# Optimization experiments

Measured on AMD Instinct MI355X. Metric: run time of the kernel, lower is better.

Reference implementation:

```python
import jax, jax.numpy as jnp
import numpy as np

B, T, D, V, N = 64, 512, 256, 32000, 48


def gru_layer(x_tbd, wx, wh, b):
    """Keras GRU (reset_after=True). x_tbd: [T,B,Din]; returns [T,B,D]."""
    bx, bh = b[0], b[1]
    px = x_tbd @ wx + bx  # [T,B,3D] precomputed input projections
    units = wh.shape[0]

    def step(h, pxt):
        ph = h @ wh + bh
        xz, xr, xh = jnp.split(pxt, 3, axis=-1)
        hz, hr, hh = jnp.split(ph, 3, axis=-1)
        z = jax.nn.sigmoid(xz + hz)
        r = jax.nn.sigmoid(xr + hr)
        hc = jnp.tanh(xh + r * hh)
        hn = z * h + (1.0 - z) * hc
        return hn, hn

    h0 = jnp.zeros((x_tbd.shape[1], units), x_tbd.dtype)
    _, out = jax.lax.scan(step, h0, px)
    return out


def crf_log_likelihood(emis, tags, seq_len, trans):
    Bb, Tt, Nn = emis.shape
    t_idx = jnp.arange(Tt)
    mask = (t_idx[None, :] < seq_len[:, None]).astype(emis.dtype)  # [B,T]
    unary = jnp.take_along_axis(emis, tags[..., None], axis=2)[..., 0]
    us = jnp.sum(unary * mask, axis=1)
    tr = trans[tags[:, :-1], tags[:, 1:]]  # [B,T-1]
    ts = jnp.sum(tr * mask[:, 1:], axis=1)

    def step(alpha, inp):
        e_t, m_t = inp  # [B,N], [B]
        new = jax.nn.logsumexp(alpha[:, :, None] + trans[None], axis=1) + e_t
        return jnp.where(m_t[:, None], new, alpha), None

    alpha, _ = jax.lax.scan(step, emis[:, 0],
                            (emis.transpose(1, 0, 2)[1:], (mask > 0).T[1:]))
    log_z = jax.nn.logsumexp(alpha, axis=-1)
    return us + ts - log_z


def crf_decode(emis, trans, seq_len):
    Bb, Tt, Nn = emis.shape
    mask = jnp.arange(Tt)[None, :] < seq_len[:, None]
    ident = jnp.arange(Nn, dtype=jnp.int32)[None, :]

    def step(alpha, inp):
        e_t, m_t = inp
        sc = alpha[:, :, None] + trans[None]  # [B,N,N] prev->cur
        bp = jnp.argmax(sc, axis=1).astype(jnp.int32)
        new = jnp.max(sc, axis=1) + e_t
        alpha_n = jnp.where(m_t[:, None], new, alpha)
        bp = jnp.where(m_t[:, None], bp, ident)
        return alpha_n, bp

    alpha, bps = jax.lax.scan(step, emis[:, 0],
                              (emis.transpose(1, 0, 2)[1:], mask.T[1:]))
    score = jnp.max(alpha, axis=-1)
    last = jnp.argmax(alpha, axis=-1).astype(jnp.int32)  # [B]

    def back(tag, bp):
        prev = jnp.take_along_axis(bp, tag[:, None], axis=1)[:, 0]
        return prev, tag

    tag0, tags = jax.lax.scan(back, last, bps, reverse=True)  # tags[i]=pos i+1
    pred = jnp.concatenate([tag0[:, None], tags.T], axis=1)  # [B,T]
    return pred, score


def setup_inputs() -> dict:
    key = jax.random.key(0)
    ks = jax.random.split(key, 20)
    s = 0.05
    inp = {
        'x': jax.random.randint(ks[0], (B, T), 0, V, dtype=jnp.int32),
        'y': jax.random.randint(ks[1], (B, T), 0, N, dtype=jnp.int32),
        'seq_len': jax.random.randint(ks[2], (B,), T // 2, T + 1, dtype=jnp.int32),
        'embed': jax.random.normal(ks[3], (V, D), jnp.float32) * s,
        'wx_f': jax.random.normal(ks[4], (D, 3 * D), jnp.float32) * s,
        'wh_f': jax.random.normal(ks[5], (D, 3 * D), jnp.float32) * s,
        'b_f': jnp.zeros((2, 3 * D), jnp.float32),
        'wx_b': jax.random.normal(ks[6], (D, 3 * D), jnp.float32) * s,
        'wh_b': jax.random.normal(ks[7], (D, 3 * D), jnp.float32) * s,
        'b_b': jnp.zeros((2, 3 * D), jnp.float32),
        'wq': jax.random.normal(ks[8], (2 * D, D), jnp.float32) * s,
        'bq': jnp.zeros((D,), jnp.float32),
        'wk': jax.random.normal(ks[9], (2 * D, D), jnp.float32) * s,
        'bk': jnp.zeros((D,), jnp.float32),
        'wv': jax.random.normal(ks[10], (2 * D, D), jnp.float32) * s,
        'bv': jnp.zeros((D,), jnp.float32),
        'wt': jax.random.normal(ks[11], (D, N), jnp.float32) * s,
        'bt': jnp.zeros((N,), jnp.float32),
        'trans': jax.random.normal(ks[12], (N, N), jnp.float32) * s,
    }
    return inp


def reference(x, y, seq_len, embed, wx_f, wh_f, b_f, wx_b, wh_b, b_b,
              wq, bq, wk, bk, wv, bv, wt, bt, trans):
    emb = embed[x]  # [B,T,D]
    xt = emb.transpose(1, 0, 2)  # [T,B,D]
    hf = gru_layer(xt, wx_f, wh_f, b_f)
    hb = gru_layer(xt[::-1], wx_b, wh_b, b_b)[::-1]
    h = jnp.concatenate([hf, hb], axis=-1).transpose(1, 0, 2)  # [B,T,2D]
    q = h @ wq + bq
    k = h @ wk + bk
    v = h @ wv + bv
    w = jax.nn.softmax(jnp.einsum('btd,bsd->bts', q, k), axis=-1)
    a = jnp.einsum('bts,bsd->btd', w, v)
    logits = a @ wt + bt  # [B,T,N]
    pred, _ = crf_decode(logits, trans, seq_len)
    ll = crf_log_likelihood(logits, y, seq_len, trans)
    return pred, ll
```

## Files before the change

### kernel.cpp

```cpp
#include <hip/hip_runtime.h>
#include <math.h>

typedef float f32;
typedef short short8 __attribute__((ext_vector_type(8)));
typedef float f32x4 __attribute__((ext_vector_type(4)));

#define TT 512
#define BB 64
#define DD 256
#define NN 48

static const size_t OFF_EBF  = 0;
static const size_t OFF_PXF  = 16384000;
static const size_t OFF_PXB  = OFF_PXF + 50331648;
static const size_t OFF_HBF_F= OFF_PXB + 50331648;
static const size_t OFF_HBF_B= OFF_HBF_F + 16777216;
static const size_t OFF_WXTF = OFF_HBF_B + 16777216;
static const size_t OFF_WXTB = OFF_WXTF + 393216;
static const size_t OFF_WHTF = OFF_WXTB + 393216;
static const size_t OFF_WHTB = OFF_WHTF + 393216;
static const size_t OFF_WQT  = OFF_WHTB + 393216;
static const size_t OFF_WKT  = OFF_WQT + 262144;
static const size_t OFF_WVT  = OFF_WKT + 262144;
static const size_t OFF_WTT  = OFF_WVT + 262144;
static const size_t OFF_QBF = OFF_PXF;
static const size_t OFF_KBF = OFF_QBF + 16777216;
static const size_t OFF_VBF = OFF_KBF + 16777216;
static const size_t OFF_VT  = OFF_VBF + 16777216;
static const size_t OFF_SCB = OFF_VT  + 16777216;
static const size_t OFF_ABF = OFF_QBF;
static const size_t OFF_LG  = OFF_KBF;

__device__ __forceinline__ ushort f2bf(f32 f) {
  union { f32 f; unsigned u; } v; v.f = f;
  unsigned r = v.u + 0x7fffu + ((v.u >> 16) & 1u);
  return (ushort)(r >> 16);
}
__device__ __forceinline__ f32 bf2f(ushort u) {
  union { unsigned u; f32 f; } v; v.u = ((unsigned)u) << 16; return v.f;
}
__device__ __forceinline__ f32 fsigmoid(f32 x) { return 1.f / (1.f + __expf(-x)); }
__device__ __forceinline__ f32 ftanh(f32 x) { return 1.f - 2.f / (__expf(2.f * x) + 1.f); }

template <int PL2>
__global__ __launch_bounds__(256) void tconv_k(
    const f32* __restrict__ in, ushort* __restrict__ out, int total, int Q) {
  int o = blockIdx.x * 256 + threadIdx.x;
  if (o >= total) return;
  int q = o >> PL2, p = o & ((1 << PL2) - 1);
  out[o] = f2bf(in[(size_t)p * Q + q]);
}

__global__ __launch_bounds__(256) void conv_embed_k(
    const f32* __restrict__ in, ushort* __restrict__ out, int n4) {
  int i = blockIdx.x * 256 + threadIdx.x;
  if (i >= n4) return;
  float4 v = ((const float4*)in)[i];
  ushort4 o;
  o.x = f2bf(v.x); o.y = f2bf(v.y); o.z = f2bf(v.z); o.w = f2bf(v.w);
  ((ushort4*)out)[i] = o;
}

__global__ __launch_bounds__(256) void tr_v_k(
    const ushort* __restrict__ in, ushort* __restrict__ out) {
  __shared__ ushort tile[32][33];
  int b = blockIdx.z;
  int s0 = blockIdx.x * 32, d0 = blockIdx.y * 32;
  int xc = threadIdx.x & 31, y0 = threadIdx.x >> 5;
  for (int yy = y0; yy < 32; yy += 8)
    tile[yy][xc] = in[((size_t)b * 512 + s0 + yy) * 256 + d0 + xc];
  __syncthreads();
  for (int yy = y0; yy < 32; yy += 8)
    out[((size_t)b * 256 + d0 + yy) * 512 + s0 + xc] = tile[xc][yy];
}

enum { GM_PX = 0, GM_QKV = 1, GM_SC = 2, GM_AV = 3, GM_LG = 4 };

template <int MODE>
__global__ __launch_bounds__(256) void mgemm(
    const ushort* __restrict__ Aa, const ushort* __restrict__ Ab,
    const ushort* __restrict__ Bt,
    f32* __restrict__ Cf, ushort* __restrict__ Cb,
    const f32* __restrict__ bias, const int* __restrict__ xi,
    int Ndim, int K, int rev) {
  const int m0 = blockIdx.y * 128;
  const int n0 = blockIdx.x * 128;
  const int bz = blockIdx.z;
  const int tid = threadIdx.x;
  const int l = tid & 63, w = tid >> 6;
  const int wr = w >> 1, wc = w & 1;
  __shared__ __align__(16) short Al[128 * 40];
  __shared__ __align__(16) short Bl[128 * 40];
  f32x4 acc[4][4] = {};

  const int rowa = tid >> 1;
  const int kha = (tid & 1) * 16;
  const int rA = m0 + rowa;
  const ushort* aBase = nullptr;
  const ushort* aBase2 = nullptr;
  if constexpr (MODE == GM_PX) {
    int tg = rA >> 6, b = rA & 63;
    int ts = rev ? (511 - tg) : tg;
    aBase = Aa + (size_t)xi[b * 512 + ts] * 256;
  } else if constexpr (MODE == GM_QKV) {
    int bl = rA >> 9, t = rA & 511;
    aBase = Aa + ((size_t)(t * 64 + bl)) * 256;
    aBase2 = Ab + ((size_t)((511 - t) * 64 + bl)) * 256;
  } else if constexpr (MODE == GM_SC) {
    aBase = Aa + ((size_t)(bz * 512 + rA)) * 256;
  } else if constexpr (MODE == GM_AV) {
    aBase = Aa + ((size_t)(bz * 512 + rA)) * 512;
  } else {
    aBase = Aa + (size_t)rA * 256;
  }
  const int rowb = tid >> 1;
  const int khb = (tid & 1) * 16;
  int rowg = n0 + rowb;
  if constexpr (MODE == GM_SC) rowg += bz * 512;
  if constexpr (MODE == GM_AV) rowg += bz * 256;
  const ushort* bBase = Bt + (size_t)rowg * K;
  const bool bValid = (MODE != GM_LG) || (n0 + rowb < Ndim);

  for (int k0 = 0; k0 < K; k0 += 32) {
    {
      int kk = k0 + kha;
      const ushort* src;
      if constexpr (MODE == GM_QKV)
        src = (kk < 256) ? aBase + kk : aBase2 + (kk - 256);
      else
        src = aBase + kk;
      uint4 a0 = *(const uint4*)src;
      uint4 a1 = *(const uint4*)(src + 8);
      *(uint4*)&Al[rowa * 40 + kha] = a0;
      *(uint4*)&Al[rowa * 40 + kha + 8] = a1;
    }
    {
      uint4 v0 = make_uint4(0, 0, 0, 0), v1 = make_uint4(0, 0, 0, 0);
      if (bValid) {
        const ushort* src = bBase + k0 + khb;
        v0 = *(const uint4*)src;
        v1 = *(const uint4*)(src + 8);
      }
      *(uint4*)&Bl[rowb * 40 + khb] = v0;
      *(uint4*)&Bl[rowb * 40 + khb + 8] = v1;
    }
    __syncthreads();
    const int fr = l & 15, fg = l >> 4;
    short8 af[4], bfr[4];
#pragma unroll
    for (int mf = 0; mf < 4; ++mf)
      af[mf] = *(const short8*)&Al[(wr * 64 + mf * 16 + fr) * 40 + fg * 8];
#pragma unroll
    for (int nf = 0; nf < 4; ++nf)
      bfr[nf] = *(const short8*)&Bl[(wc * 64 + nf * 16 + fr) * 40 + fg * 8];
#pragma unroll
    for (int mf = 0; mf < 4; ++mf)
#pragma unroll
      for (int nf = 0; nf < 4; ++nf)
        acc[mf][nf] = __builtin_amdgcn_mfma_f32_16x16x32_bf16(
            af[mf], bfr[nf], acc[mf][nf], 0, 0, 0);
    __syncthreads();
  }

  const int fr = l & 15, fq = l >> 4;
#pragma unroll
  for (int mf = 0; mf < 4; ++mf) {
#pragma unroll
    for (int nf = 0; nf < 4; ++nf) {
      int col = n0 + wc * 64 + nf * 16 + fr;
      f32 bs = 0.f;
      if (bias && col < Ndim) bs = bias[col];
#pragma unroll
      for (int rg = 0; rg < 4; ++rg) {
        int row = m0 + wr * 64 + mf * 16 + fq * 4 + rg;
        f32 vv = acc[mf][nf][rg] + bs;
        if constexpr (MODE == GM_PX) {
          int tg = row >> 6, b = row & 63;
          int gate = col >> 8, hc = col & 255;
          int rg4b = b >> 4, lr = b & 15;
          size_t idx = (size_t)tg * 49152 + (size_t)rg4b * 12288 +
                       (size_t)gate * 4096 + (size_t)(hc >> 4) * 256 +
                       (hc & 15) * 16 + (lr >> 2) * 4 + (lr & 3);
          Cb[idx] = f2bf(vv);
        } else if constexpr (MODE == GM_QKV)
          Cb[(size_t)row * 256 + col] = f2bf(vv);
        else if constexpr (MODE == GM_SC)
          Cb[((size_t)bz * 512 + row) * 512 + col] = f2bf(vv);
        else if constexpr (MODE == GM_AV)
          Cb[((size_t)bz * 512 + row) * 256 + col] = f2bf(vv);
        else {
          if (col < Ndim) Cf[(size_t)row * 48 + col] = vv;
        }
      }
    }
  }
}

#define MFMA_B16 __builtin_amdgcn_mfma_f32_16x16x32_bf16

#define PXLOAD(T, P) {                                         \
  size_t tb_ = (size_t)(T) * 49152;                            \
  P##0 = *(const uint2*)(px + tb_ + offp);                     \
  P##1 = *(const uint2*)(px + tb_ + offp + 4096);              \
  P##2 = *(const uint2*)(px + tb_ + offp + 8192);              \
}

#define GATE1(RI, UZ, UR, UH)                                  \
{                                                              \
  f32 zv_ = fsigmoid(az[RI] + bhz + bf2f((ushort)(UZ)));       \
  f32 rv_ = fsigmoid(ar[RI] + bhr + bf2f((ushort)(UR)));       \
  f32 hc_ = ftanh(bf2f((ushort)(UH)) + rv_ * (ah[RI] + bhh));  \
  f32 hn_ = zv_ * h0##RI + (1.f - zv_) * hc_;                  \
  h0##RI = hn_;                                                \
  *(ushort*)&dst_[(kb0 * 16 + fq * 4 + (RI)) * 16 + e2] = f2bf(hn_); \
}

#define STEP(T, BUF, PC, PN) {                                 \
  if ((T) + 1 < TT) PXLOAD((T) + 1, PN);                       \
  if ((T) > 0) {                                               \
    uint2 v_ = *(const uint2*)&ldsH[BUF][(ckb * 16 + crow) * 16 + chalf * 8]; \
    *(uint2*)&hseq[(((size_t)(T) - 1) * 64 + rowbase + crow) * 256 + ckb * 8 + chalf * 4] = v_; \
  }                                                            \
  uint2 q0_ = PC##0, q1_ = PC##1, q2_ = PC##2;                 \
  f32x4 az = {}, ar = {}, ah = {};                             \
  _Pragma("unroll")                                            \
  for (int ks = 0; ks < 8; ++ks) {                             \
    short8 a_  = *(const short8*)&ldsH[BUF][((ks * 4 + fq) * 16 + fr) * 16]; \
    short8 wh8 = *(const short8*)&ldsWh[wcol * 512 + ((ks * 64 + fq * 16) ^ ((wcol & 7) << 6))]; \
    az = MFMA_B16(a_, wz[ks], az, 0, 0, 0);                    \
    ar = MFMA_B16(a_, wrg[ks], ar, 0, 0, 0);                   \
    ah = MFMA_B16(a_, wh8, ah, 0, 0, 0);                       \
  }                                                            \
  char* dst_ = ldsH[(BUF) ^ 1];                                \
  GATE1(0, q0_.x,       q1_.x,       q2_.x)                    \
  GATE1(1, q0_.x >> 16, q1_.x >> 16, q2_.x >> 16)              \
  GATE1(2, q0_.y,       q1_.y,       q2_.y)                    \
  GATE1(3, q0_.y >> 16, q1_.y >> 16, q2_.y >> 16)              \
  __syncthreads();                                             \
}

__global__ __launch_bounds__(1024, 4) void gru_scan8(
    const ushort* __restrict__ pxf, const ushort* __restrict__ pxb,
    const ushort* __restrict__ whtf, const ushort* __restrict__ whtb,
    const f32* __restrict__ b_f, const f32* __restrict__ b_b,
    ushort* __restrict__ hfbf, ushort* __restrict__ hbbf) {
  const int dir = blockIdx.x >> 2;
  const int rg4 = blockIdx.x & 3;
  const int tid = threadIdx.x;
  const int w = tid >> 6, l = tid & 63;
  const int fr = l & 15, fq = l >> 4;
  const ushort* pxd = dir ? pxb : pxf;
  const ushort* wht = dir ? whtb : whtf;
  const f32* bh = (dir ? b_b : b_f) + 768;
  ushort* hseq = dir ? hbbf : hfbf;

  __shared__ __align__(16) char ldsWh[131072];
  __shared__ __align__(16) char ldsH[2][8192];

#pragma unroll
  for (int i = 0; i < 8; ++i) {
    int idx = i * 1024 + tid;
    int col = idx >> 5, kc = idx & 31;
    uint4 v = *(const uint4*)&wht[(size_t)(512 + col) * 256 + kc * 8];
    *(uint4*)&ldsWh[col * 512 + ((kc * 16) ^ ((col & 7) << 6))] = v;
  }
  if (tid < 512) ((uint4*)ldsH[0])[tid] = make_uint4(0, 0, 0, 0);

  const int wcol = w * 16 + fr;
  short8 wz[8], wrg[8];
#pragma unroll
  for (int ks = 0; ks < 8; ++ks) {
    wz[ks]  = *(const short8*)&wht[(size_t)wcol * 256 + ks * 32 + fq * 8];
    wrg[ks] = *(const short8*)&wht[(size_t)(256 + wcol) * 256 + ks * 32 + fq * 8];
  }
  const f32 bhz = bh[wcol], bhr = bh[256 + wcol], bhh = bh[512 + wcol];
  f32 h00 = 0.f, h01 = 0.f, h02 = 0.f, h03 = 0.f;

  const ushort* px = pxd + (size_t)rg4 * 12288;
  const int offp = w * 256 + fr * 16 + fq * 4;
  const int rowbase = rg4 * 16;
  const int kb0 = wcol >> 3;
  const int e2 = (wcol & 7) * 2;
  const int ckb = (tid >> 1) >> 4;
  const int crow = (tid >> 1) & 15;
  const int chalf = tid & 1;

  uint2 pA0, pA1, pA2;
  uint2 pB0, pB1, pB2;
  PXLOAD(0, pA);
  __syncthreads();

#pragma unroll 1
  for (int t2 = 0; t2 < TT; t2 += 2) {
    STEP(t2, 0, pA, pB);
    STEP(t2 + 1, 1, pB, pA);
  }
  {
    uint2 v = *(const uint2*)&ldsH[0][(ckb * 16 + crow) * 16 + chalf * 8];
    *(uint2*)&hseq[((size_t)511 * 64 + rowbase + crow) * 256 + ckb * 8 + chalf * 4] = v;
  }
}

__global__ __launch_bounds__(256) void softmax_ip(ushort* __restrict__ p) {
  size_t row = blockIdx.x;
  uint* pr = (uint*)(p + row * 512);
  int tid = threadIdx.x;
  uint u = pr[tid];
  f32 v0 = bf2f((ushort)(u & 0xffff)), v1 = bf2f((ushort)(u >> 16));
  f32 m = fmaxf(v0, v1);
  for (int off = 32; off; off >>= 1) m = fmaxf(m, __shfl_xor(m, off));
  __shared__ f32 red[4];
  __shared__ f32 red2[4];
  if ((tid & 63) == 0) red[tid >> 6] = m;
  __syncthreads();
  m = fmaxf(fmaxf(red[0], red[1]), fmaxf(red[2], red[3]));
  f32 e0 = __expf(v0 - m), e1 = __expf(v1 - m);
  f32 s = e0 + e1;
  for (int off = 32; off; off >>= 1) s += __shfl_xor(s, off);
  if ((tid & 63) == 0) red2[tid >> 6] = s;
  __syncthreads();
  s = red2[0] + red2[1] + red2[2] + red2[3];
  f32 inv = 1.f / s;
  pr[tid] = (uint)f2bf(e0 * inv) | ((uint)f2bf(e1 * inv) << 16);
}

__global__ __launch_bounds__(64) void crf_ll_k(
    const f32* __restrict__ logits, const int* __restrict__ y,
    const int* __restrict__ seq_len, const f32* __restrict__ trans,
    f32* __restrict__ out) {
  const int b = blockIdx.x, tid = threadIdx.x;
  __shared__ f32 tr[NN * NN];
  for (int i = tid; i < NN * NN; i += 64) tr[i] = trans[i];
  const f32* em = logits + (size_t)b * TT * NN;
  const int L = seq_len[b];
  const bool act = tid < NN;
  f32 Ecol[NN];
#pragma unroll
  for (int i = 0; i < NN; ++i)
    Ecol[i] = act ? __expf(trans[i * NN + tid]) : 0.f;
  f32 alpha = act ? em[tid] : -1e30f;
  __syncthreads();
  for (int t = 1; t < L; ++t) {
    f32 m = alpha;
    for (int off = 32; off; off >>= 1) m = fmaxf(m, __shfl_xor(m, off));
    f32 e = __expf(alpha - m);
    f32 s = 0.f;
#pragma unroll
    for (int i = 0; i < NN; ++i) s += __shfl(e, i) * Ecol[i];
    if (act) alpha = m + __logf(s) + em[t * NN + tid];
  }
  f32 us = 0.f, ts = 0.f;
  for (int t = tid; t < TT; t += 64) {
    if (t < L) {
      us += em[t * NN + y[b * TT + t]];
      if (t >= 1) ts += tr[y[b * TT + t - 1] * NN + y[b * TT + t]];
    }
  }
  for (int off = 32; off; off >>= 1) { us += __shfl_xor(us, off); ts += __shfl_xor(ts, off); }
  f32 m = alpha;
  for (int off = 32; off; off >>= 1) m = fmaxf(m, __shfl_xor(m, off));
  f32 e = __expf(alpha - m);
  f32 s = e;
  for (int off = 32; off; off >>= 1) s += __shfl_xor(s, off);
  if (tid == 0) out[(size_t)BB * TT + b] = us + ts - (m + __logf(s));
}

__global__ __launch_bounds__(64) void crf_decode_k(
    const f32* __restrict__ logits, const int* __restrict__ seq_len,
    const f32* __restrict__ trans, f32* __restrict__ out) {
  const int b = blockIdx.x, tid = threadIdx.x;
  __shared__ f32 tr[NN][NN];
  __shared__ f32 al[2][NN];
  __shared__ unsigned char bp[TT - 1][NN];
  __shared__ unsigned char pr[TT];
  for (int i = tid; i < NN * NN; i += 64) tr[i / NN][i % NN] = trans[i];
  const f32* em = logits + (size_t)b * TT * NN;
  const int L = seq_len[b];
  if (tid < NN) al[0][tid] = em[tid];
  __syncthreads();
  int cur = 0;
  for (int t = 1; t < TT; ++t) {
    if (tid < NN) {
      if (t < L) {
        f32 m = -1e30f; int arg = 0;
        for (int i = 0; i < NN; ++i) {
          f32 v = al[cur][i] + tr[i][tid];
          if (v > m) { m = v; arg = i; }
        }
        al[cur ^ 1][tid] = m + em[t * NN + tid];
        bp[t - 1][tid] = (unsigned char)arg;
      } else {
        al[cur ^ 1][tid] = al[cur][tid];
        bp[t - 1][tid] = (unsigned char)tid;
      }
    }
    __syncthreads();
    cur ^= 1;
  }
  if (tid == 0) {
    f32 m = -1e30f; int last = 0;
    for (int i = 0; i < NN; ++i)
      if (al[cur][i] > m) { m = al[cur][i]; last = i; }
    int tag = last;
    for (int t = TT - 2; t >= 0; --t) { pr[t + 1] = (unsigned char)tag; tag = bp[t][tag]; }
    pr[0] = (unsigned char)tag;
  }
  __syncthreads();
  for (int t = tid; t < TT; t += 64)
    out[(size_t)b * TT + t] = (f32)pr[t];
}

extern "C" void kernel_launch(void* const* d_in, const int* in_sizes, int n_in,
                              void* d_out, int out_size, void* d_ws, size_t ws_size,
                              hipStream_t stream) {
  const int* x       = (const int*)d_in[0];
  const int* y       = (const int*)d_in[1];
  const int* seq_len = (const int*)d_in[2];
  const f32* embed   = (const f32*)d_in[3];
  const f32* wx_f    = (const f32*)d_in[4];
  const f32* wh_f    = (const f32*)d_in[5];
  const f32* b_f     = (const f32*)d_in[6];
  const f32* wx_b    = (const f32*)d_in[7];
  const f32* wh_b    = (const f32*)d_in[8];
  const f32* b_b     = (const f32*)d_in[9];
  const f32* wq      = (const f32*)d_in[10];
  const f32* bq      = (const f32*)d_in[11];
  const f32* wk      = (const f32*)d_in[12];
  const f32* bk      = (const f32*)d_in[13];
  const f32* wv      = (const f32*)d_in[14];
  const f32* bv      = (const f32*)d_in[15];
  const f32* wt      = (const f32*)d_in[16];
  const f32* bt      = (const f32*)d_in[17];
  const f32* trans   = (const f32*)d_in[18];
  f32* out = (f32*)d_out;

  char* ws = (char*)d_ws;
  ushort* ebf  = (ushort*)(ws + OFF_EBF);
  ushort* pxfb = (ushort*)(ws + OFF_PXF);
  ushort* pxbb = (ushort*)(ws + OFF_PXB);
  ushort* hfbf = (ushort*)(ws + OFF_HBF_F);
  ushort* hbbf = (ushort*)(ws + OFF_HBF_B);
  ushort* wxtf = (ushort*)(ws + OFF_WXTF);
  ushort* wxtb = (ushort*)(ws + OFF_WXTB);
  ushort* whtf = (ushort*)(ws + OFF_WHTF);
  ushort* whtb = (ushort*)(ws + OFF_WHTB);
  ushort* wqt  = (ushort*)(ws + OFF_WQT);
  ushort* wkt  = (ushort*)(ws + OFF_WKT);
  ushort* wvt  = (ushort*)(ws + OFF_WVT);
  ushort* wtt  = (ushort*)(ws + OFF_WTT);
  ushort* qbf = (ushort*)(ws + OFF_QBF);
  ushort* kbf = (ushort*)(ws + OFF_KBF);
  ushort* vbf = (ushort*)(ws + OFF_VBF);
  ushort* vT  = (ushort*)(ws + OFF_VT);
  ushort* scb = (ushort*)(ws + OFF_SCB);
  ushort* abf = (ushort*)(ws + OFF_ABF);
  f32*    lg  = (f32*)(ws + OFF_LG);

  conv_embed_k<<<8000, 256, 0, stream>>>(embed, ebf, 2048000);
  tconv_k<8><<<768, 256, 0, stream>>>(wx_f, wxtf, 196608, 768);
  tconv_k<8><<<768, 256, 0, stream>>>(wx_b, wxtb, 196608, 768);
  tconv_k<8><<<768, 256, 0, stream>>>(wh_f, whtf, 196608, 768);
  tconv_k<8><<<768, 256, 0, stream>>>(wh_b, whtb, 196608, 768);
  tconv_k<9><<<512, 256, 0, stream>>>(wq, wqt, 131072, 256);
  tconv_k<9><<<512, 256, 0, stream>>>(wk, wkt, 131072, 256);
  tconv_k<9><<<512, 256, 0, stream>>>(wv, wvt, 131072, 256);
  tconv_k<8><<<48, 256, 0, stream>>>(wt, wtt, 12288, 48);

  mgemm<GM_PX><<<dim3(6, 256), 256, 0, stream>>>(
      ebf, nullptr, wxtf, nullptr, pxfb, b_f, x, 768, 256, 0);
  mgemm<GM_PX><<<dim3(6, 256), 256, 0, stream>>>(
      ebf, nullptr, wxtb, nullptr, pxbb, b_b, x, 768, 256, 1);
  gru_scan8<<<8, 1024, 0, stream>>>(pxfb, pxbb, whtf, whtb, b_f, b_b, hfbf, hbbf);

  mgemm<GM_QKV><<<dim3(2, 256), 256, 0, stream>>>(
      hfbf, hbbf, wqt, nullptr, qbf, bq, nullptr, 256, 512, 0);
  mgemm<GM_QKV><<<dim3(2, 256), 256, 0, stream>>>(
      hfbf, hbbf, wkt, nullptr, kbf, bk, nullptr, 256, 512, 0);
  mgemm<GM_QKV><<<dim3(2, 256), 256, 0, stream>>>(
      hfbf, hbbf, wvt, nullptr, vbf, bv, nullptr, 256, 512, 0);
  tr_v_k<<<dim3(16, 8, 64), 256, 0, stream>>>(vbf, vT);
  mgemm<GM_SC><<<dim3(4, 4, 64), 256, 0, stream>>>(
      qbf, nullptr, kbf, nullptr, scb, nullptr, nullptr, 512, 256, 0);
  softmax_ip<<<BB * TT, 256, 0, stream>>>(scb);
  mgemm<GM_AV><<<dim3(2, 4, 64), 256, 0, stream>>>(
      scb, nullptr, vT, nullptr, abf, nullptr, nullptr, 256, 512, 0);
  mgemm<GM_LG><<<dim3(1, 256), 256, 0, stream>>>(
      abf, nullptr, wtt, lg, nullptr, bt, nullptr, 48, 256, 0);

  crf_ll_k<<<BB, 64, 0, stream>>>(lg, y, seq_len, trans, out);
  crf_decode_k<<<BB, 64, 0, stream>>>(lg, seq_len, trans, out);
}
```

Baseline: 2.755 ms.

## Keep all GRU recurrent weights in registers with 512-thread scan blocks

The GRU scan kernel drops from 1024 to 512 threads per block, and each wave now covers two 16-column tiles. All three gate weight slices (z, r, h) are held in registers, which removes the 128KB LDS copy of the candidate-gate weights and its per-step LDS reads. The input-projection layout written by the PX GEMM is reordered so each thread loads one 16-byte vector per gate, and the h-sequence writeback uses 16-byte stores. The old one-step-ahead prefetch of projections is removed. This raises register pressure and halves the wave count available to hide latency in the serial recurrence.

```diff
diff --git a/kernel.cpp b/kernel.cpp
--- a/kernel.cpp
+++ b/kernel.cpp
@@ -177,10 +177,11 @@
         if constexpr (MODE == GM_PX) {
           int tg = row >> 6, b = row & 63;
           int gate = col >> 8, hc = col & 255;
+          int wv2 = hc >> 5, ctb2 = (hc >> 4) & 1, frb = hc & 15;
           int rg4b = b >> 4, lr = b & 15;
           size_t idx = (size_t)tg * 49152 + (size_t)rg4b * 12288 +
-                       (size_t)gate * 4096 + (size_t)(hc >> 4) * 256 +
-                       (hc & 15) * 16 + (lr >> 2) * 4 + (lr & 3);
+                       (size_t)gate * 4096 + (size_t)wv2 * 512 +
+                       frb * 32 + (lr >> 2) * 8 + ctb2 * 4 + (lr & 3);
           Cb[idx] = f2bf(vv);
         } else if constexpr (MODE == GM_QKV)
           Cb[(size_t)row * 256 + col] = f2bf(vv);
@@ -198,48 +199,49 @@
 
 #define MFMA_B16 __builtin_amdgcn_mfma_f32_16x16x32_bf16
 
-#define PXLOAD(T, P) {                                         \
-  size_t tb_ = (size_t)(T) * 49152;                            \
-  P##0 = *(const uint2*)(px + tb_ + offp);                     \
-  P##1 = *(const uint2*)(px + tb_ + offp + 4096);              \
-  P##2 = *(const uint2*)(px + tb_ + offp + 8192);              \
-}
-
-#define GATE1(RI, UZ, UR, UH)                                  \
+#define GATE1(CT, RI, UZ, UR, UH, AZ, AR, AH, KB)              \
 {                                                              \
-  f32 zv_ = fsigmoid(az[RI] + bhz + bf2f((ushort)(UZ)));       \
-  f32 rv_ = fsigmoid(ar[RI] + bhr + bf2f((ushort)(UR)));       \
-  f32 hc_ = ftanh(bf2f((ushort)(UH)) + rv_ * (ah[RI] + bhh));  \
-  f32 hn_ = zv_ * h0##RI + (1.f - zv_) * hc_;                  \
-  h0##RI = hn_;                                                \
-  *(ushort*)&dst_[(kb0 * 16 + fq * 4 + (RI)) * 16 + e2] = f2bf(hn_); \
-}
-
-#define STEP(T, BUF, PC, PN) {                                 \
-  if ((T) + 1 < TT) PXLOAD((T) + 1, PN);                       \
+  f32 zv_ = fsigmoid((AZ)[RI] + bhz##CT + bf2f((ushort)(UZ))); \
+  f32 rv_ = fsigmoid((AR)[RI] + bhr##CT + bf2f((ushort)(UR))); \
+  f32 hc_ = ftanh(bf2f((ushort)(UH)) + rv_ * ((AH)[RI] + bhh##CT)); \
+  f32 hn_ = zv_ * h##CT##RI + (1.f - zv_) * hc_;               \
+  h##CT##RI = hn_;                                             \
+  *(ushort*)&dst_[(((KB) * 16) + fq * 4 + (RI)) * 16 + e2] = f2bf(hn_); \
+}
+
+#define STEP(T, BUF) {                                         \
+  const ushort* pt_ = px + (size_t)(T) * 49152;                \
+  uint4 q0_ = *(const uint4*)(pt_ + offp);                     \
+  uint4 q1_ = *(const uint4*)(pt_ + offp + 4096);              \
+  uint4 q2_ = *(const uint4*)(pt_ + offp + 8192);              \
   if ((T) > 0) {                                               \
-    uint2 v_ = *(const uint2*)&ldsH[BUF][(ckb * 16 + crow) * 16 + chalf * 8]; \
-    *(uint2*)&hseq[(((size_t)(T) - 1) * 64 + rowbase + crow) * 256 + ckb * 8 + chalf * 4] = v_; \
+    uint4 v_ = *(const uint4*)&ldsH[BUF][((ckb * 16) + crow) * 16]; \
+    *(uint4*)&hseq[(((size_t)(T) - 1) * 64 + rowbase + crow) * 256 + ckb * 8] = v_; \
   }                                                            \
-  uint2 q0_ = PC##0, q1_ = PC##1, q2_ = PC##2;                 \
-  f32x4 az = {}, ar = {}, ah = {};                             \
+  f32x4 az0 = {}, az1 = {}, ar0 = {}, ar1 = {}, ah0 = {}, ah1 = {}; \
   _Pragma("unroll")                                            \
   for (int ks = 0; ks < 8; ++ks) {                             \
-    short8 a_  = *(const short8*)&ldsH[BUF][((ks * 4 + fq) * 16 + fr) * 16]; \
-    short8 wh8 = *(const short8*)&ldsWh[wcol * 512 + ((ks * 64 + fq * 16) ^ ((wcol & 7) << 6))]; \
-    az = MFMA_B16(a_, wz[ks], az, 0, 0, 0);                    \
-    ar = MFMA_B16(a_, wrg[ks], ar, 0, 0, 0);                   \
-    ah = MFMA_B16(a_, wh8, ah, 0, 0, 0);                       \
+    short8 a_ = *(const short8*)&ldsH[BUF][((ks * 4 + fq) * 16 + fr) * 16]; \
+    az0 = MFMA_B16(a_, wz0[ks], az0, 0, 0, 0);                 \
+    ar0 = MFMA_B16(a_, wr0[ks], ar0, 0, 0, 0);                 \
+    ah0 = MFMA_B16(a_, wh0[ks], ah0, 0, 0, 0);                 \
+    az1 = MFMA_B16(a_, wz1[ks], az1, 0, 0, 0);                 \
+    ar1 = MFMA_B16(a_, wr1[ks], ar1, 0, 0, 0);                 \
+    ah1 = MFMA_B16(a_, wh1[ks], ah1, 0, 0, 0);                 \
   }                                                            \
   char* dst_ = ldsH[(BUF) ^ 1];                                \
-  GATE1(0, q0_.x,       q1_.x,       q2_.x)                    \
-  GATE1(1, q0_.x >> 16, q1_.x >> 16, q2_.x >> 16)              \
-  GATE1(2, q0_.y,       q1_.y,       q2_.y)                    \
-  GATE1(3, q0_.y >> 16, q1_.y >> 16, q2_.y >> 16)              \
+  GATE1(0, 0, q0_.x,       q1_.x,       q2_.x,       az0, ar0, ah0, kb0) \
+  GATE1(0, 1, q0_.x >> 16, q1_.x >> 16, q2_.x >> 16, az0, ar0, ah0, kb0) \
+  GATE1(0, 2, q0_.y,       q1_.y,       q2_.y,       az0, ar0, ah0, kb0) \
+  GATE1(0, 3, q0_.y >> 16, q1_.y >> 16, q2_.y >> 16, az0, ar0, ah0, kb0) \
+  GATE1(1, 0, q0_.z,       q1_.z,       q2_.z,       az1, ar1, ah1, kb1) \
+  GATE1(1, 1, q0_.z >> 16, q1_.z >> 16, q2_.z >> 16, az1, ar1, ah1, kb1) \
+  GATE1(1, 2, q0_.w,       q1_.w,       q2_.w,       az1, ar1, ah1, kb1) \
+  GATE1(1, 3, q0_.w >> 16, q1_.w >> 16, q2_.w >> 16, az1, ar1, ah1, kb1) \
   __syncthreads();                                             \
 }
 
-__global__ __launch_bounds__(1024, 4) void gru_scan8(
+__global__ __launch_bounds__(512, 2) void gru_scan9(
     const ushort* __restrict__ pxf, const ushort* __restrict__ pxb,
     const ushort* __restrict__ whtf, const ushort* __restrict__ whtb,
     const f32* __restrict__ b_f, const f32* __restrict__ b_b,
@@ -254,50 +256,47 @@
   const f32* bh = (dir ? b_b : b_f) + 768;
   ushort* hseq = dir ? hbbf : hfbf;
 
-  __shared__ __align__(16) char ldsWh[131072];
   __shared__ __align__(16) char ldsH[2][8192];
 
-#pragma unroll
-  for (int i = 0; i < 8; ++i) {
-    int idx = i * 1024 + tid;
-    int col = idx >> 5, kc = idx & 31;
-    uint4 v = *(const uint4*)&wht[(size_t)(512 + col) * 256 + kc * 8];
-    *(uint4*)&ldsWh[col * 512 + ((kc * 16) ^ ((col & 7) << 6))] = v;
-  }
   if (tid < 512) ((uint4*)ldsH[0])[tid] = make_uint4(0, 0, 0, 0);
 
-  const int wcol = w * 16 + fr;
-  short8 wz[8], wrg[8];
+  const int c0 = w * 32 + fr;
+  const int c1 = w * 32 + 16 + fr;
+  short8 wz0[8], wz1[8], wr0[8], wr1[8], wh0[8], wh1[8];
 #pragma unroll
   for (int ks = 0; ks < 8; ++ks) {
-    wz[ks]  = *(const short8*)&wht[(size_t)wcol * 256 + ks * 32 + fq * 8];
-    wrg[ks] = *(const short8*)&wht[(size_t)(256 + wcol) * 256 + ks * 32 + fq * 8];
-  }
-  const f32 bhz = bh[wcol], bhr = bh[256 + wcol], bhh = bh[512 + wcol];
+    wz0[ks] = *(const short8*)&wht[(size_t)c0 * 256 + ks * 32 + fq * 8];
+    wz1[ks] = *(const short8*)&wht[(size_t)c1 * 256 + ks * 32 + fq * 8];
+    wr0[ks] = *(const short8*)&wht[(size_t)(256 + c0) * 256 + ks * 32 + fq * 8];
+    wr1[ks] = *(const short8*)&wht[(size_t)(256 + c1) * 256 + ks * 32 + fq * 8];
+    wh0[ks] = *(const short8*)&wht[(size_t)(512 + c0) * 256 + ks * 32 + fq * 8];
+    wh1[ks] = *(const short8*)&wht[(size_t)(512 + c1) * 256 + ks * 32 + fq * 8];
+  }
+  const f32 bhz0 = bh[c0], bhz1 = bh[c1];
+  const f32 bhr0 = bh[256 + c0], bhr1 = bh[256 + c1];
+  const f32 bhh0 = bh[512 + c0], bhh1 = bh[512 + c1];
   f32 h00 = 0.f, h01 = 0.f, h02 = 0.f, h03 = 0.f;
+  f32 h10 = 0.f, h11 = 0.f, h12 = 0.f, h13 = 0.f;
 
   const ushort* px = pxd + (size_t)rg4 * 12288;
-  const int offp = w * 256 + fr * 16 + fq * 4;
+  const int offp = w * 512 + fr * 32 + fq * 8;
   const int rowbase = rg4 * 16;
-  const int kb0 = wcol >> 3;
-  const int e2 = (wcol & 7) * 2;
-  const int ckb = (tid >> 1) >> 4;
-  const int crow = (tid >> 1) & 15;
-  const int chalf = tid & 1;
-
-  uint2 pA0, pA1, pA2;
-  uint2 pB0, pB1, pB2;
-  PXLOAD(0, pA);
+  const int kb0 = w * 4 + (fr >> 3);
+  const int kb1 = kb0 + 2;
+  const int e2 = (fr & 7) * 2;
+  const int ckb = tid & 31;
+  const int crow = tid >> 5;
+
   __syncthreads();
 
 #pragma unroll 1
   for (int t2 = 0; t2 < TT; t2 += 2) {
-    STEP(t2, 0, pA, pB);
-    STEP(t2 + 1, 1, pB, pA);
+    STEP(t2, 0);
+    STEP(t2 + 1, 1);
   }
   {
-    uint2 v = *(const uint2*)&ldsH[0][(ckb * 16 + crow) * 16 + chalf * 8];
-    *(uint2*)&hseq[((size_t)511 * 64 + rowbase + crow) * 256 + ckb * 8 + chalf * 4] = v;
+    uint4 v = *(const uint4*)&ldsH[0][((ckb * 16) + crow) * 16];
+    *(uint4*)&hseq[((size_t)511 * 64 + rowbase + crow) * 256 + ckb * 8] = v;
   }
 }
 
@@ -470,7 +469,7 @@
       ebf, nullptr, wxtf, nullptr, pxfb, b_f, x, 768, 256, 0);
   mgemm<GM_PX><<<dim3(6, 256), 256, 0, stream>>>(
       ebf, nullptr, wxtb, nullptr, pxbb, b_b, x, 768, 256, 1);
-  gru_scan8<<<8, 1024, 0, stream>>>(pxfb, pxbb, whtf, whtb, b_f, b_b, hfbf, hbbf);
+  gru_scan9<<<8, 512, 0, stream>>>(pxfb, pxbb, whtf, whtb, b_f, b_b, hfbf, hbbf);
 
   mgemm<GM_QKV><<<dim3(2, 256), 256, 0, stream>>>(
       hfbf, hbbf, wqt, nullptr, qbf, bq, nullptr, 256, 512, 0);
```

After: 2.732 ms. About the same (-0.8%).
